# Performance work log

Measured on AMD Instinct MI355X. Metric: run time of the kernel, lower is better.

## Reference

```python
import jax, jax.numpy as jnp
import numpy as np

B, C, H, W = 4, 3, 1024, 1024
RADII = (8, 16, 32, 64)
EPS = 1e-5  # BatchNorm2d default eps


def _box_sum(x, r, s):
    # depthwise all-ones conv (kernel r, stride s, VALID padding) == summed box
    return jax.lax.reduce_window(x, 0.0, jax.lax.add, (1, 1, r, r), (1, 1, s, s), 'VALID')


def _axis_interp_ac(x, n_out, axis):
    # bilinear (align_corners=True) interpolation along one axis
    n_in = x.shape[axis]
    pos = jnp.arange(n_out, dtype=x.dtype) * ((n_in - 1) / max(n_out - 1, 1))
    i0 = jnp.clip(jnp.floor(pos).astype(jnp.int32), 0, n_in - 2)
    w = pos - i0.astype(x.dtype)
    a = jnp.take(x, i0, axis=axis)
    b = jnp.take(x, i0 + 1, axis=axis)
    shape = [1] * x.ndim
    shape[axis] = n_out
    w = w.reshape(shape)
    return a * (1 - w) + b * w


def _resize_ac(x, oh, ow):
    x = _axis_interp_ac(x, oh, 2)
    x = _axis_interp_ac(x, ow, 3)
    return x


def _bn(x, g, b, rm, rv):
    inv = g / jnp.sqrt(rv + EPS)
    return x * inv[None, :, None, None] + (b - rm * inv)[None, :, None, None]


def _forward(guide, src, w1, g1, b1, rm1, rv1, w2, g2, b2, rm2, rv2, w3):
    Hg, Wg = guide.shape[2], guide.shape[3]
    gg = guide * guide
    gs = guide * src
    ones = jnp.ones((1, guide.shape[1], Hg, Wg), guide.dtype)
    stats = []
    for r in RADII:
        s = r // 2
        N = _box_sum(ones, r, s)
        mx = _box_sum(guide, r, s) / N
        my = _box_sum(src, r, s) / N
        cov = _box_sum(gs, r, s) / N - mx * my
        var = _box_sum(gg, r, s) / N - mx * mx
        stats.append((mx, my, cov, var))
    mx1, my1, cov1, var1 = stats[0]
    oh, ow = cov1.shape[2], cov1.shape[3]
    feats = [cov1, var1]
    for (_, _, cov, var) in stats[1:]:
        feats.append(_resize_ac(cov, oh, ow))
        feats.append(_resize_ac(var, oh, ow))
    x = jnp.concatenate(feats, axis=1)  # [B,24,oh,ow]
    x = jax.nn.relu(_bn(jnp.einsum('oc,bchw->bohw', w1, x), g1, b1, rm1, rv1))
    x = jax.nn.relu(_bn(jnp.einsum('oc,bchw->bohw', w2, x), g2, b2, rm2, rv2))
    A = jnp.einsum('oc,bchw->bohw', w3, x)  # [B,3,oh,ow]
    bb = my1 - A * mx1
    mean_A = _resize_ac(A, Hg, Wg)
    mean_b = _resize_ac(bb, Hg, Wg)
    return mean_A * guide + mean_b


def setup_inputs() -> dict:
    key = jax.random.key(0)
    ks = jax.random.split(key, 5)
    f32 = jnp.float32
    return {
        'guide': jax.random.normal(ks[0], (B, C, H, W), f32),
        'src': jax.random.normal(ks[1], (B, C, H, W), f32),
        'w1': jax.random.normal(ks[2], (48, 24), f32) * 0.05,
        'g1': jnp.ones((48,), f32), 'b1': jnp.zeros((48,), f32),
        'rm1': jnp.zeros((48,), f32), 'rv1': jnp.ones((48,), f32),
        'w2': jax.random.normal(ks[3], (48, 48), f32) * 0.05,
        'g2': jnp.ones((48,), f32), 'b2': jnp.zeros((48,), f32),
        'rm2': jnp.zeros((48,), f32), 'rv2': jnp.ones((48,), f32),
        'w3': jax.random.normal(ks[4], (3, 48), f32) * 0.05,
    }


def reference(guide, src, w1, g1, b1, rm1, rv1, w2, g2, b2, rm2, rv2, w3):
    return _forward(guide, src, w1, g1, b1, rm1, rv1, w2, g2, b2, rm2, rv2, w3)
```

## Files before the change

### kernel.cpp

```cpp
#include <hip/hip_runtime.h>

#define HH 1024
#define WW 1024
#define NB 4
#define NC 3
#define BC 12
#define N1 255
#define N2 127
#define N3 63
#define N4 31
#define EPS 1e-5f

constexpr size_t S8_OFF  = 0;
constexpr size_t S8_SZ   = 4ull * BC * N1 * N1;
constexpr size_t S16_OFF = S8_OFF + S8_SZ;
constexpr size_t S16_SZ  = 4ull * BC * N2 * N2;
constexpr size_t S32_OFF = S16_OFF + S16_SZ;
constexpr size_t S32_SZ  = 4ull * BC * N3 * N3;
constexpr size_t S64_OFF = S32_OFF + S32_SZ;
constexpr size_t S64_SZ  = 4ull * BC * N4 * N4;
constexpr size_t CV16_OFF = S64_OFF + S64_SZ;
constexpr size_t CV16_SZ  = 2ull * BC * N2 * N2;
constexpr size_t CV32_OFF = CV16_OFF + CV16_SZ;
constexpr size_t CV32_SZ  = 2ull * BC * N3 * N3;
constexpr size_t CV64_OFF = CV32_OFF + CV32_SZ;
constexpr size_t CV64_SZ  = 2ull * BC * N4 * N4;
constexpr size_t A_OFF    = CV64_OFF + CV64_SZ;
constexpr size_t A_SZ     = (size_t)NB * NC * N1 * N1;
constexpr size_t BB_OFF   = A_OFF + A_SZ;
constexpr size_t WF_OFF   = BB_OFF + A_SZ;
constexpr int WF_W1T = 0;
constexpr int WF_B1  = 1152;
constexpr int WF_W2T = 1200;
constexpr int WF_B2  = 3504;
constexpr int WF_W3T = 3552;

__global__ __launch_bounds__(256) void prep_kernel(
    const float* __restrict__ w1, const float* __restrict__ g1,
    const float* __restrict__ b1, const float* __restrict__ rm1,
    const float* __restrict__ rv1,
    const float* __restrict__ w2, const float* __restrict__ g2,
    const float* __restrict__ b2, const float* __restrict__ rm2,
    const float* __restrict__ rv2,
    const float* __restrict__ w3, float* __restrict__ Wf)
{
    __shared__ float i1[48], i2[48];
    int t = threadIdx.x;
    if (t < 48) {
        float iv = g1[t] * rsqrtf(rv1[t] + EPS);
        i1[t] = iv;
        Wf[WF_B1 + t] = b1[t] - rm1[t] * iv;
        float iw = g2[t] * rsqrtf(rv2[t] + EPS);
        i2[t] = iw;
        Wf[WF_B2 + t] = b2[t] - rm2[t] * iw;
    }
    __syncthreads();
    for (int k = t; k < 48 * 24; k += 256) {
        int o = k / 24, c = k % 24;
        Wf[WF_W1T + c * 48 + o] = w1[k] * i1[o];
    }
    for (int k = t; k < 48 * 48; k += 256) {
        int o = k / 48, c = k % 48;
        Wf[WF_W2T + c * 48 + o] = w2[k] * i2[o];
    }
    for (int k = t; k < 3 * 48; k += 256) {
        int c = k / 48, kk = k % 48;
        Wf[WF_W3T + kk * 3 + c] = w3[k];
    }
}

__global__ __launch_bounds__(256) void base_kernel(
    const float* __restrict__ guide, const float* __restrict__ src,
    float* __restrict__ S8)
{
    int blk = blockIdx.x;
    int bc  = blk / N1;
    int i   = blk % N1;
    int j   = threadIdx.x;
    if (j >= N1) return;

    const float* g0 = guide + (size_t)bc * HH * WW + (size_t)(4 * i) * WW + 4 * j;
    const float* s0 = src   + (size_t)bc * HH * WW + (size_t)(4 * i) * WW + 4 * j;

    float sg = 0.f, ss = 0.f, sgg = 0.f, sgs = 0.f;
#pragma unroll
    for (int r = 0; r < 8; ++r) {
        float4 ga = *(const float4*)(g0 + (size_t)r * WW);
        float4 gb = *(const float4*)(g0 + (size_t)r * WW + 4);
        float4 sa = *(const float4*)(s0 + (size_t)r * WW);
        float4 sb = *(const float4*)(s0 + (size_t)r * WW + 4);
        float ge[8] = {ga.x, ga.y, ga.z, ga.w, gb.x, gb.y, gb.z, gb.w};
        float se[8] = {sa.x, sa.y, sa.z, sa.w, sb.x, sb.y, sb.z, sb.w};
#pragma unroll
        for (int k = 0; k < 8; ++k) {
            float g = ge[k], s = se[k];
            sg  += g;
            ss  += s;
            sgg += g * g;
            sgs += g * s;
        }
    }
    size_t qs  = (size_t)BC * N1 * N1;
    size_t idx = (size_t)bc * N1 * N1 + (size_t)i * N1 + j;
    S8[0 * qs + idx] = sg;
    S8[1 * qs + idx] = ss;
    S8[2 * qs + idx] = sgg;
    S8[3 * qs + idx] = sgs;
}

__global__ __launch_bounds__(256) void pyr_kernel(
    const float* __restrict__ Sin, float* __restrict__ Sout,
    float* __restrict__ CVout, int nin, int nout, float invN)
{
    int idx = blockIdx.x * blockDim.x + threadIdx.x;
    int total = BC * nout * nout;
    if (idx >= total) return;
    int j  = idx % nout;
    int t  = idx / nout;
    int i  = t % nout;
    int bc = t / nout;

    size_t sIn  = (size_t)BC * nin * nin;
    size_t base = (size_t)bc * nin * nin;
    int p = 2 * i, q = 2 * j;

    float sums[4];
#pragma unroll
    for (int qt = 0; qt < 4; ++qt) {
        const float* P = Sin + (size_t)qt * sIn + base;
        sums[qt] = P[(size_t)p * nin + q] + P[(size_t)(p + 2) * nin + q] +
                   P[(size_t)p * nin + q + 2] + P[(size_t)(p + 2) * nin + q + 2];
    }
    size_t sOut = (size_t)BC * nout * nout;
    size_t o    = (size_t)bc * nout * nout + (size_t)i * nout + j;
    Sout[0 * sOut + o] = sums[0];
    Sout[1 * sOut + o] = sums[1];
    Sout[2 * sOut + o] = sums[2];
    Sout[3 * sOut + o] = sums[3];
    float mx = sums[0] * invN, my = sums[1] * invN;
    CVout[o]        = sums[3] * invN - mx * my;
    CVout[sOut + o] = sums[2] * invN - mx * mx;
}

__global__ __launch_bounds__(256) void mlp_kernel(
    const float* __restrict__ S8,
    const float* __restrict__ CV16, const float* __restrict__ CV32,
    const float* __restrict__ CV64,
    const float* __restrict__ Wf,
    float* __restrict__ A, float* __restrict__ Bb)
{
    const float* __restrict__ W1T = Wf + WF_W1T;
    const float* __restrict__ B1  = Wf + WF_B1;
    const float* __restrict__ W2T = Wf + WF_W2T;
    const float* __restrict__ B2  = Wf + WF_B2;
    const float* __restrict__ W3T = Wf + WF_W3T;

    int idx = blockIdx.x * 256 + threadIdx.x;
    if (idx >= NB * N1 * N1) return;
    int ox = idx % N1;
    int r  = idx / N1;
    int oy = r % N1;
    int b  = r / N1;

    float feats[24], mx1[3], my1[3];

    size_t s8q = (size_t)BC * N1 * N1;
#pragma unroll
    for (int c = 0; c < 3; ++c) {
        size_t o = (size_t)(b * 3 + c) * N1 * N1 + (size_t)oy * N1 + ox;
        float sg = S8[o], ss = S8[s8q + o], sgg = S8[2 * s8q + o], sgs = S8[3 * s8q + o];
        float mx = sg * (1.f / 64.f), my = ss * (1.f / 64.f);
        mx1[c] = mx; my1[c] = my;
        feats[c]     = sgs * (1.f / 64.f) - mx * my;
        feats[3 + c] = sgg * (1.f / 64.f) - mx * mx;
    }

    const float* CVs[3] = {CV16, CV32, CV64};
    const int nins[3]   = {N2, N3, N4};
    const float scales[3] = {(float)(126.0 / 254.0), (float)(62.0 / 254.0),
                             (float)(30.0 / 254.0)};
#pragma unroll
    for (int l = 0; l < 3; ++l) {
        const float* CV = CVs[l];
        int nin = nins[l];
        float sc = scales[l];
        float py = (float)oy * sc;
        int   i0 = min(max((int)floorf(py), 0), nin - 2);
        float wy = py - (float)i0;
        float px = (float)ox * sc;
        int   j0 = min(max((int)floorf(px), 0), nin - 2);
        float wx = px - (float)j0;
        size_t cvq = (size_t)BC * nin * nin;
        int fo = 6 + 6 * l;
#pragma unroll
        for (int c = 0; c < 3; ++c) {
            size_t bix = (size_t)(b * 3 + c) * nin * nin;
            size_t o00 = bix + (size_t)i0 * nin + j0;
            float c00 = CV[o00], c01 = CV[o00 + 1];
            float c10 = CV[o00 + nin], c11 = CV[o00 + nin + 1];
            feats[fo + c] = (c00 * (1.f - wy) + c10 * wy) * (1.f - wx) +
                            (c01 * (1.f - wy) + c11 * wy) * wx;
            float v00 = CV[cvq + o00], v01 = CV[cvq + o00 + 1];
            float v10 = CV[cvq + o00 + nin], v11 = CV[cvq + o00 + nin + 1];
            feats[fo + 3 + c] = (v00 * (1.f - wy) + v10 * wy) * (1.f - wx) +
                                (v01 * (1.f - wy) + v11 * wy) * wx;
        }
    }

    float acc1[48];
#pragma unroll
    for (int o = 0; o < 48; ++o) acc1[o] = B1[o];
#pragma unroll
    for (int c = 0; c < 24; ++c) {
        float f = feats[c];
#pragma unroll
        for (int o = 0; o < 48; ++o) acc1[o] = fmaf(W1T[c * 48 + o], f, acc1[o]);
    }
    float h1[48];
#pragma unroll
    for (int o = 0; o < 48; ++o) h1[o] = fmaxf(acc1[o], 0.f);

    float acc2[48];
#pragma unroll
    for (int o = 0; o < 48; ++o) acc2[o] = B2[o];
#pragma unroll
    for (int c = 0; c < 48; ++c) {
        float f = h1[c];
#pragma unroll
        for (int o = 0; o < 48; ++o) acc2[o] = fmaf(W2T[c * 48 + o], f, acc2[o]);
    }

    float a3[3] = {0.f, 0.f, 0.f};
#pragma unroll
    for (int o = 0; o < 48; ++o) {
        float h2 = fmaxf(acc2[o], 0.f);
#pragma unroll
        for (int c = 0; c < 3; ++c) a3[c] = fmaf(W3T[o * 3 + c], h2, a3[c]);
    }

#pragma unroll
    for (int c = 0; c < 3; ++c) {
        size_t o = (size_t)(b * 3 + c) * N1 * N1 + (size_t)oy * N1 + ox;
        A[o]  = a3[c];
        Bb[o] = my1[c] - a3[c] * mx1[c];
    }
}

__global__ __launch_bounds__(256) void final_kernel(
    const float* __restrict__ guide, const float* __restrict__ A,
    const float* __restrict__ Bb, float* __restrict__ out)
{
    __shared__ float aH[N1 + 1], bH[N1 + 1];
    int blk = blockIdx.x;
    int bc  = blk / HH;
    int h   = blk % HH;

    const float scale = (float)(254.0 / 1023.0);
    float py = (float)h * scale;
    int   i0 = min(max((int)floorf(py), 0), N1 - 2);
    float wy = py - (float)i0;

    int t = threadIdx.x;
    if (t < N1) {
        size_t base = (size_t)bc * N1 * N1 + (size_t)i0 * N1 + t;
        aH[t] = A[base] * (1.f - wy) + A[base + N1] * wy;
        bH[t] = Bb[base] * (1.f - wy) + Bb[base + N1] * wy;
    }
    __syncthreads();

    const float* gp = guide + (size_t)bc * HH * WW + (size_t)h * WW;
    float*       op = out   + (size_t)bc * HH * WW + (size_t)h * WW;

    float4 g4 = *(const float4*)(gp + 4 * t);
    float4 o4;
    float ge[4] = {g4.x, g4.y, g4.z, g4.w};
    float oe[4];
#pragma unroll
    for (int k = 0; k < 4; ++k) {
        int w = 4 * t + k;
        float px = (float)w * scale;
        int   j0 = min(max((int)floorf(px), 0), N1 - 2);
        float wx = px - (float)j0;
        float a = aH[j0] * (1.f - wx) + aH[j0 + 1] * wx;
        float bbv = bH[j0] * (1.f - wx) + bH[j0 + 1] * wx;
        oe[k] = a * ge[k] + bbv;
    }
    o4.x = oe[0]; o4.y = oe[1]; o4.z = oe[2]; o4.w = oe[3];
    *(float4*)(op + 4 * t) = o4;
}

extern "C" void kernel_launch(void* const* d_in, const int* in_sizes, int n_in,
                              void* d_out, int out_size, void* d_ws, size_t ws_size,
                              hipStream_t stream)
{
    const float* guide = (const float*)d_in[0];
    const float* src   = (const float*)d_in[1];
    const float* w1    = (const float*)d_in[2];
    const float* g1    = (const float*)d_in[3];
    const float* b1    = (const float*)d_in[4];
    const float* rm1   = (const float*)d_in[5];
    const float* rv1   = (const float*)d_in[6];
    const float* w2    = (const float*)d_in[7];
    const float* g2    = (const float*)d_in[8];
    const float* b2    = (const float*)d_in[9];
    const float* rm2   = (const float*)d_in[10];
    const float* rv2   = (const float*)d_in[11];
    const float* w3    = (const float*)d_in[12];
    float*       out   = (float*)d_out;

    float* ws   = (float*)d_ws;
    float* S8   = ws + S8_OFF;
    float* S16  = ws + S16_OFF;
    float* S32  = ws + S32_OFF;
    float* S64  = ws + S64_OFF;
    float* CV16 = ws + CV16_OFF;
    float* CV32 = ws + CV32_OFF;
    float* CV64 = ws + CV64_OFF;
    float* Abuf = ws + A_OFF;
    float* Bbuf = ws + BB_OFF;
    float* Wf   = ws + WF_OFF;

    prep_kernel<<<1, 256, 0, stream>>>(w1, g1, b1, rm1, rv1, w2, g2, b2, rm2, rv2,
                                       w3, Wf);

    base_kernel<<<BC * N1, 256, 0, stream>>>(guide, src, S8);

    {
        int total = BC * N2 * N2;
        pyr_kernel<<<(total + 255) / 256, 256, 0, stream>>>(S8, S16, CV16, N1, N2,
                                                            1.f / 256.f);
    }
    {
        int total = BC * N3 * N3;
        pyr_kernel<<<(total + 255) / 256, 256, 0, stream>>>(S16, S32, CV32, N2, N3,
                                                            1.f / 1024.f);
    }
    {
        int total = BC * N4 * N4;
        pyr_kernel<<<(total + 255) / 256, 256, 0, stream>>>(S32, S64, CV64, N3, N4,
                                                            1.f / 4096.f);
    }

    {
        int total = NB * N1 * N1;
        mlp_kernel<<<(total + 255) / 256, 256, 0, stream>>>(
            S8, CV16, CV32, CV64, Wf, Abuf, Bbuf);
    }

    final_kernel<<<BC * HH, 256, 0, stream>>>(guide, Abuf, Bbuf, out);
}
```

Before: 234.2 us.

## Split MLP hidden channels across two threads per pixel via LDS

The per-pixel MLP kernel now uses two threads per pixel, each computing half of the 48 hidden channels. Layer-1 activations are exchanged through shared memory (padded stride 51), and the two partial layer-3 sums are combined through shared memory as well. The goal is to cut per-thread register pressure (48-wide accumulators become 24-wide) and raise occupancy, with launch bounds set to 6 waves. The cost is two block barriers, LDS traffic, and feature gathering repeated by both threads of a pixel.

```diff
diff --git a/kernel.cpp b/kernel.cpp
--- a/kernel.cpp
+++ b/kernel.cpp
@@ -142,7 +142,7 @@
     CVout[sOut + o] = sums[2] * invN - mx * mx;
 }
 
-__global__ __launch_bounds__(256) void mlp_kernel(
+__global__ __launch_bounds__(256, 6) void mlp_kernel(
     const float* __restrict__ S8,
     const float* __restrict__ CV16, const float* __restrict__ CV32,
     const float* __restrict__ CV64,
@@ -155,94 +155,124 @@
     const float* __restrict__ B2  = Wf + WF_B2;
     const float* __restrict__ W3T = Wf + WF_W3T;
 
-    int idx = blockIdx.x * 256 + threadIdx.x;
-    if (idx >= NB * N1 * N1) return;
-    int ox = idx % N1;
-    int r  = idx / N1;
-    int oy = r % N1;
-    int b  = r / N1;
-
-    float feats[24], mx1[3], my1[3];
-
-    size_t s8q = (size_t)BC * N1 * N1;
-#pragma unroll
-    for (int c = 0; c < 3; ++c) {
-        size_t o = (size_t)(b * 3 + c) * N1 * N1 + (size_t)oy * N1 + ox;
-        float sg = S8[o], ss = S8[s8q + o], sgg = S8[2 * s8q + o], sgs = S8[3 * s8q + o];
-        float mx = sg * (1.f / 64.f), my = ss * (1.f / 64.f);
-        mx1[c] = mx; my1[c] = my;
-        feats[c]     = sgs * (1.f / 64.f) - mx * my;
-        feats[3 + c] = sgg * (1.f / 64.f) - mx * mx;
-    }
-
-    const float* CVs[3] = {CV16, CV32, CV64};
-    const int nins[3]   = {N2, N3, N4};
-    const float scales[3] = {(float)(126.0 / 254.0), (float)(62.0 / 254.0),
-                             (float)(30.0 / 254.0)};
-#pragma unroll
-    for (int l = 0; l < 3; ++l) {
-        const float* CV = CVs[l];
-        int nin = nins[l];
-        float sc = scales[l];
-        float py = (float)oy * sc;
-        int   i0 = min(max((int)floorf(py), 0), nin - 2);
-        float wy = py - (float)i0;
-        float px = (float)ox * sc;
-        int   j0 = min(max((int)floorf(px), 0), nin - 2);
-        float wx = px - (float)j0;
-        size_t cvq = (size_t)BC * nin * nin;
-        int fo = 6 + 6 * l;
+    __shared__ float HLDS[128 * 51];
+
+    int t  = threadIdx.x;
+    int pl = t & 127;
+    int hf = t >> 7;
+    int ob = 24 * hf;
+
+    int pixel = blockIdx.x * 128 + pl;
+    bool act  = pixel < NB * N1 * N1;
+
+    size_t obase = 0;
+    float mx1[3], my1[3], a3p[3] = {0.f, 0.f, 0.f};
+
+    if (act) {
+        int ox = pixel % N1;
+        int r  = pixel / N1;
+        int oy = r % N1;
+        int b  = r / N1;
+        obase = (size_t)(b * 3) * N1 * N1 + (size_t)oy * N1 + ox;
+
+        float feats[24];
+
+        size_t s8q = (size_t)BC * N1 * N1;
 #pragma unroll
         for (int c = 0; c < 3; ++c) {
-            size_t bix = (size_t)(b * 3 + c) * nin * nin;
-            size_t o00 = bix + (size_t)i0 * nin + j0;
-            float c00 = CV[o00], c01 = CV[o00 + 1];
-            float c10 = CV[o00 + nin], c11 = CV[o00 + nin + 1];
-            feats[fo + c] = (c00 * (1.f - wy) + c10 * wy) * (1.f - wx) +
-                            (c01 * (1.f - wy) + c11 * wy) * wx;
-            float v00 = CV[cvq + o00], v01 = CV[cvq + o00 + 1];
-            float v10 = CV[cvq + o00 + nin], v11 = CV[cvq + o00 + nin + 1];
-            feats[fo + 3 + c] = (v00 * (1.f - wy) + v10 * wy) * (1.f - wx) +
-                                (v01 * (1.f - wy) + v11 * wy) * wx;
-        }
-    }
-
-    float acc1[48];
-#pragma unroll
-    for (int o = 0; o < 48; ++o) acc1[o] = B1[o];
-#pragma unroll
-    for (int c = 0; c < 24; ++c) {
-        float f = feats[c];
-#pragma unroll
-        for (int o = 0; o < 48; ++o) acc1[o] = fmaf(W1T[c * 48 + o], f, acc1[o]);
-    }
-    float h1[48];
-#pragma unroll
-    for (int o = 0; o < 48; ++o) h1[o] = fmaxf(acc1[o], 0.f);
-
-    float acc2[48];
-#pragma unroll
-    for (int o = 0; o < 48; ++o) acc2[o] = B2[o];
-#pragma unroll
-    for (int c = 0; c < 48; ++c) {
-        float f = h1[c];
-#pragma unroll
-        for (int o = 0; o < 48; ++o) acc2[o] = fmaf(W2T[c * 48 + o], f, acc2[o]);
-    }
-
-    float a3[3] = {0.f, 0.f, 0.f};
-#pragma unroll
-    for (int o = 0; o < 48; ++o) {
-        float h2 = fmaxf(acc2[o], 0.f);
-#pragma unroll
-        for (int c = 0; c < 3; ++c) a3[c] = fmaf(W3T[o * 3 + c], h2, a3[c]);
-    }
-
-#pragma unroll
-    for (int c = 0; c < 3; ++c) {
-        size_t o = (size_t)(b * 3 + c) * N1 * N1 + (size_t)oy * N1 + ox;
-        A[o]  = a3[c];
-        Bb[o] = my1[c] - a3[c] * mx1[c];
+            size_t o = obase + (size_t)c * N1 * N1;
+            float sg = S8[o], ss = S8[s8q + o];
+            float sgg = S8[2 * s8q + o], sgs = S8[3 * s8q + o];
+            float mx = sg * (1.f / 64.f), my = ss * (1.f / 64.f);
+            mx1[c] = mx; my1[c] = my;
+            feats[c]     = sgs * (1.f / 64.f) - mx * my;
+            feats[3 + c] = sgg * (1.f / 64.f) - mx * mx;
+        }
+
+        const float* CVs[3] = {CV16, CV32, CV64};
+        const int nins[3]   = {N2, N3, N4};
+        const float scales[3] = {(float)(126.0 / 254.0), (float)(62.0 / 254.0),
+                                 (float)(30.0 / 254.0)};
+#pragma unroll
+        for (int l = 0; l < 3; ++l) {
+            const float* CV = CVs[l];
+            int nin = nins[l];
+            float sc = scales[l];
+            float py = (float)oy * sc;
+            int   i0 = min(max((int)floorf(py), 0), nin - 2);
+            float wy = py - (float)i0;
+            float px = (float)ox * sc;
+            int   j0 = min(max((int)floorf(px), 0), nin - 2);
+            float wx = px - (float)j0;
+            size_t cvq = (size_t)BC * nin * nin;
+            int fo = 6 + 6 * l;
+#pragma unroll
+            for (int c = 0; c < 3; ++c) {
+                size_t bix = (size_t)(b * 3 + c) * nin * nin;
+                size_t o00 = bix + (size_t)i0 * nin + j0;
+                float c00 = CV[o00], c01 = CV[o00 + 1];
+                float c10 = CV[o00 + nin], c11 = CV[o00 + nin + 1];
+                feats[fo + c] = (c00 * (1.f - wy) + c10 * wy) * (1.f - wx) +
+                                (c01 * (1.f - wy) + c11 * wy) * wx;
+                float v00 = CV[cvq + o00], v01 = CV[cvq + o00 + 1];
+                float v10 = CV[cvq + o00 + nin], v11 = CV[cvq + o00 + nin + 1];
+                feats[fo + 3 + c] = (v00 * (1.f - wy) + v10 * wy) * (1.f - wx) +
+                                    (v01 * (1.f - wy) + v11 * wy) * wx;
+            }
+        }
+
+        float acc1[24];
+#pragma unroll
+        for (int o = 0; o < 24; ++o) acc1[o] = B1[ob + o];
+#pragma unroll
+        for (int c = 0; c < 24; ++c) {
+            float f = feats[c];
+#pragma unroll
+            for (int o = 0; o < 24; ++o)
+                acc1[o] = fmaf(W1T[c * 48 + ob + o], f, acc1[o]);
+        }
+#pragma unroll
+        for (int o = 0; o < 24; ++o)
+            HLDS[pl * 51 + ob + o] = fmaxf(acc1[o], 0.f);
+    }
+
+    __syncthreads();
+
+    if (act) {
+        float acc2[24];
+#pragma unroll
+        for (int o = 0; o < 24; ++o) acc2[o] = B2[ob + o];
+#pragma unroll
+        for (int c = 0; c < 48; ++c) {
+            float f = HLDS[pl * 51 + c];
+#pragma unroll
+            for (int o = 0; o < 24; ++o)
+                acc2[o] = fmaf(W2T[c * 48 + ob + o], f, acc2[o]);
+        }
+
+#pragma unroll
+        for (int kk = 0; kk < 24; ++kk) {
+            float h2 = fmaxf(acc2[kk], 0.f);
+#pragma unroll
+            for (int cc = 0; cc < 3; ++cc)
+                a3p[cc] = fmaf(W3T[(ob + kk) * 3 + cc], h2, a3p[cc]);
+        }
+        if (hf) {
+#pragma unroll
+            for (int cc = 0; cc < 3; ++cc) HLDS[pl * 51 + 48 + cc] = a3p[cc];
+        }
+    }
+
+    __syncthreads();
+
+    if (act && hf == 0) {
+#pragma unroll
+        for (int cc = 0; cc < 3; ++cc) {
+            float a = a3p[cc] + HLDS[pl * 51 + 48 + cc];
+            size_t o = obase + (size_t)cc * N1 * N1;
+            A[o]  = a;
+            Bb[o] = my1[cc] - a * mx1[cc];
+        }
     }
 }
 
@@ -342,8 +372,9 @@
     }
 
     {
-        int total = NB * N1 * N1;
-        mlp_kernel<<<(total + 255) / 256, 256, 0, stream>>>(
+        int total  = NB * N1 * N1;
+        int blocks = (total + 127) / 128;
+        mlp_kernel<<<blocks, 256, 0, stream>>>(
             S8, CV16, CV32, CV64, Wf, Abuf, Bbuf);
     }
 
```

Measured after the change: 330.4 us. 41.1% more time.
